# Optimization experiments

Hardware: AMD Instinct MI355X
Metric: run time of the kernel (lower is better)

Reference implementation:

```python
import jax, jax.numpy as jnp
import numpy as np

B, T, D, H, L, V, CTX = 4, 2048, 256, 8, 12, 256, 2048
HD = D // H


def _ln(x, w, b, eps=1e-5):
    m = x.mean(-1, keepdims=True)
    v = ((x - m) ** 2).mean(-1, keepdims=True)
    return (x - m) * jax.lax.rsqrt(v + eps) * w + b


def setup_inputs() -> dict:
    key = jax.random.key(0)
    ks = jax.random.split(key, 16)
    s = 0.02
    inp = {
        "x": jax.random.randint(ks[0], (B, T), 0, V, dtype=jnp.int32),
        "tok_embed": jax.random.normal(ks[1], (V, D), jnp.float32) * s,
        "pos_embed": jax.random.normal(ks[2], (CTX, D), jnp.float32) * s,
        # stacked per-layer params (leading axis = layer)
        "ln1_w": jnp.ones((L, D), jnp.float32),
        "ln1_b": jnp.zeros((L, D), jnp.float32),
        "qkv_w": jax.random.normal(ks[3], (L, D, 3 * D), jnp.float32) * s,
        "qkv_b": jnp.zeros((L, 3 * D), jnp.float32),
        "out_w": jax.random.normal(ks[4], (L, D, D), jnp.float32) * s,
        "out_b": jnp.zeros((L, D), jnp.float32),
        "ln2_w": jnp.ones((L, D), jnp.float32),
        "ln2_b": jnp.zeros((L, D), jnp.float32),
        "fc1_w": jax.random.normal(ks[5], (L, D, 4 * D), jnp.float32) * s,
        "fc1_b": jnp.zeros((L, 4 * D), jnp.float32),
        "fc2_w": jax.random.normal(ks[6], (L, 4 * D, D), jnp.float32) * s,
        "fc2_b": jnp.zeros((L, D), jnp.float32),
        "lnf_w": jnp.ones((D,), jnp.float32),
        "lnf_b": jnp.zeros((D,), jnp.float32),
        "head_w": jax.random.normal(ks[7], (D, V), jnp.float32) * s,
        "head_b": jnp.zeros((V,), jnp.float32),
    }
    return inp


def _forward(x, tok_embed, pos_embed, ln1_w, ln1_b, qkv_w, qkv_b, out_w, out_b,
             ln2_w, ln2_b, fc1_w, fc1_b, fc2_w, fc2_b, lnf_w, lnf_b, head_w, head_b):
    Tcur = x.shape[1]
    h = tok_embed[x] + pos_embed[:Tcur][None, :, :]  # (B,T,D)
    causal = jnp.triu(jnp.ones((Tcur, Tcur), bool), k=1)  # True above diagonal
    scale = jnp.sqrt(jnp.asarray(HD, h.dtype))

    def step(h, p):
        (l1w, l1b, qw, qb, ow, ob, l2w, l2b, f1w, f1b, f2w, f2b) = p
        # attention
        z = _ln(h, l1w, l1b)
        qkv = z @ qw + qb  # (B,T,3D)
        qkv = qkv.reshape(h.shape[0], Tcur, 3, H, HD)
        q, k, v = qkv[:, :, 0], qkv[:, :, 1], qkv[:, :, 2]  # (B,T,H,HD)
        attn = jnp.einsum('bqhd,bkhd->bhqk', q, k) / scale
        attn = jnp.where(causal, -jnp.inf, attn)
        attn = jax.nn.softmax(attn, axis=-1)
        o = jnp.einsum('bhqk,bkhd->bqhd', attn, v).reshape(h.shape[0], Tcur, D)
        h = h + o @ ow + ob
        # MLP (torch nn.GELU default = exact erf gelu)
        z = _ln(h, l2w, l2b)
        z = jax.nn.gelu(z @ f1w + f1b, approximate=False)
        h = h + z @ f2w + f2b
        return h, None

    params = (ln1_w, ln1_b, qkv_w, qkv_b, out_w, out_b,
              ln2_w, ln2_b, fc1_w, fc1_b, fc2_w, fc2_b)
    h, _ = jax.lax.scan(step, h, params)
    h = _ln(h, lnf_w, lnf_b)
    return h @ head_w + head_b  # (B,T,V)


def reference(x, tok_embed, pos_embed, ln1_w, ln1_b, qkv_w, qkv_b, out_w, out_b,
              ln2_w, ln2_b, fc1_w, fc1_b, fc2_w, fc2_b, lnf_w, lnf_b, head_w, head_b):
    return _forward(x, tok_embed, pos_embed, ln1_w, ln1_b, qkv_w, qkv_b, out_w, out_b,
                    ln2_w, ln2_b, fc1_w, fc1_b, fc2_w, fc2_b, lnf_w, lnf_b, head_w, head_b)
```

## Files before the change

kernel.cpp:

```cpp
#include <hip/hip_runtime.h>
#include <cstdint>

#define TT 2048
#define DD 256
#define HH 8
#define LL 12

typedef __attribute__((ext_vector_type(8))) short s16x8;
typedef __attribute__((ext_vector_type(4))) float f32x4;

__device__ __forceinline__ unsigned short f2bf(float f) {
  union { float f; unsigned u; } v; v.f = f;
  return (unsigned short)((v.u + 0x7FFFu + ((v.u >> 16) & 1u)) >> 16);
}

__device__ __forceinline__ unsigned cvtpk(float lo, float hi) {
  unsigned r;
  asm("v_cvt_pk_bf16_f32 %0, %1, %2" : "=v"(r) : "v"(lo), "v"(hi));
  return r;
}

__device__ __forceinline__ float geluf(float x) {
  return 0.5f * x * (1.0f + erff(x * 0.70710678118654752f));
}

__device__ __forceinline__ float fexp2(float x) {
  float r;
  asm("v_exp_f32 %0, %1" : "=v"(r) : "v"(x));
  return r;
}

__device__ __forceinline__ void gload16(const void* g, void* l) {
  __builtin_amdgcn_global_load_lds((const __attribute__((address_space(1))) unsigned int*)g,
                                   (__attribute__((address_space(3))) unsigned int*)l, 16, 0, 0);
}

__global__ __launch_bounds__(256) void k_embed(const int* __restrict__ x,
                                               const float* __restrict__ tok,
                                               const float* __restrict__ pos,
                                               float* __restrict__ h) {
  int i = blockIdx.x * 256 + threadIdx.x;
  int row = i >> 6, c = i & 63;
  int t = x[row];
  f32x4 tv = ((const f32x4*)(tok + (size_t)t * DD))[c];
  f32x4 pv = ((const f32x4*)(pos + (size_t)(row & (TT - 1)) * DD))[c];
  ((f32x4*)(h + (size_t)row * DD))[c] = tv + pv;
}

__global__ __launch_bounds__(256) void k_ln(const float* __restrict__ h,
                                            const float* __restrict__ wgt,
                                            const float* __restrict__ bia,
                                            unsigned short* __restrict__ z) {
  int row = blockIdx.x * 4 + (threadIdx.x >> 6);
  int lane = threadIdx.x & 63;
  f32x4 v = ((const f32x4*)(h + (size_t)row * DD))[lane];
  float s = v[0] + v[1] + v[2] + v[3];
#pragma unroll
  for (int m = 32; m; m >>= 1) s += __shfl_xor(s, m);
  float mean = s * (1.0f / DD);
  f32x4 d = v - mean;
  float s2 = d[0] * d[0] + d[1] * d[1] + d[2] * d[2] + d[3] * d[3];
#pragma unroll
  for (int m = 32; m; m >>= 1) s2 += __shfl_xor(s2, m);
  float inv = rsqrtf(s2 * (1.0f / DD) + 1e-5f);
  f32x4 wv = ((const f32x4*)wgt)[lane];
  f32x4 bv = ((const f32x4*)bia)[lane];
  float o0 = d[0] * inv * wv[0] + bv[0], o1 = d[1] * inv * wv[1] + bv[1];
  float o2 = d[2] * inv * wv[2] + bv[2], o3 = d[3] * inv * wv[3] + bv[3];
  unsigned long long u64 = (unsigned long long)cvtpk(o0, o1) |
                           ((unsigned long long)cvtpk(o2, o3) << 32);
  *(unsigned long long*)(z + (size_t)row * DD + lane * 4) = u64;
}

__global__ __launch_bounds__(256) void k_cast_all(const float* __restrict__ qw, const float* __restrict__ ow,
                                                  const float* __restrict__ f1, const float* __restrict__ f2,
                                                  unsigned short* __restrict__ dst) {
  __shared__ float Tt[32][33];
  const int l = blockIdx.y;
  const int t = blockIdx.x;
  const float* src;
  unsigned short* d;
  int K, N, tk, tn;
  if (t < 192) {
    src = qw + (size_t)l * 196608; d = dst + (size_t)l * 786432;
    K = 256; N = 768; tk = t / 24; tn = t % 24;
  } else if (t < 256) {
    int t2 = t - 192;
    src = ow + (size_t)l * 65536; d = dst + (size_t)l * 786432 + 196608;
    K = 256; N = 256; tk = t2 >> 3; tn = t2 & 7;
  } else if (t < 512) {
    int t3 = t - 256;
    src = f1 + (size_t)l * 262144; d = dst + (size_t)l * 786432 + 262144;
    K = 256; N = 1024; tk = t3 >> 5; tn = t3 & 31;
  } else {
    int t4 = t - 512;
    src = f2 + (size_t)l * 262144; d = dst + (size_t)l * 786432 + 524288;
    K = 1024; N = 256; tk = t4 >> 3; tn = t4 & 7;
  }
  const int tx = threadIdx.x & 31, ty = threadIdx.x >> 5;
#pragma unroll
  for (int r = 0; r < 4; ++r) {
    int row = ty + r * 8;
    Tt[row][tx] = src[(size_t)(tk * 32 + row) * N + tn * 32 + tx];
  }
  __syncthreads();
#pragma unroll
  for (int r = 0; r < 4; ++r) {
    int row = ty + r * 8;
    d[(size_t)(tn * 32 + row) * K + tk * 32 + tx] = f2bf(Tt[tx][row]);
  }
}

__global__ __launch_bounds__(256) void k_cast_tr4(const float* __restrict__ qw, const float* __restrict__ ow,
                                                  const float* __restrict__ f1, const float* __restrict__ f2,
                                                  unsigned short* __restrict__ dq, unsigned short* __restrict__ dO,
                                                  unsigned short* __restrict__ d1, unsigned short* __restrict__ d2) {
  int t0 = blockIdx.x * 256 + threadIdx.x;
  int stride = gridDim.x * 256;
  for (int i = t0; i < 196608; i += stride) dq[i] = f2bf(qw[(i & 255) * 768 + (i >> 8)]);
  for (int i = t0; i < 65536; i += stride) dO[i] = f2bf(ow[(i & 255) * 256 + (i >> 8)]);
  for (int i = t0; i < 262144; i += stride) d1[i] = f2bf(f1[(i & 255) * 1024 + (i >> 8)]);
  for (int i = t0; i < 262144; i += stride) d2[i] = f2bf(f2[(i & 1023) * 256 + (i >> 10)]);
}

__global__ __launch_bounds__(256) void k_cast_tr256(const float* __restrict__ src, unsigned short* __restrict__ dst) {
  int i = blockIdx.x * 256 + threadIdx.x;
  dst[i] = f2bf(src[(i & 255) * 256 + (i >> 8)]);
}

template <int MODE, int MI>
__global__ __launch_bounds__(256, 2) void k_gemm(const unsigned short* __restrict__ A,
                                                 const unsigned short* __restrict__ BT,
                                                 const float* __restrict__ bias,
                                                 void* out, const float* resid,
                                                 int M, int N, int K) {
  __shared__ __align__(16) unsigned short As[2][MI * 32 * 64];
  __shared__ __align__(16) unsigned short Bs[2][128 * 64];
  const int tid = threadIdx.x;
  const int lane = tid & 63, wv = tid >> 6;
  const int wr = wv >> 1, wc = wv & 1;
  const int l15 = lane & 15, g = lane >> 4;
  const int BM = MI * 32;
  const int tm = blockIdx.y, tn = blockIdx.x;
  f32x4 acc[MI][4] = {};
  const int nk = K >> 6;
  const unsigned short* Ag0 = A + (size_t)tm * BM * K;
  const unsigned short* Bg0 = BT + (size_t)tn * 128 * K;
  const int srow = tid >> 3, spart = tid & 7;

#pragma unroll
  for (int it = 0; it < MI; ++it)
    gload16(Ag0 + (size_t)(it * 32 + srow) * K + spart * 8, As[0] + (it * 256 + tid) * 8);
#pragma unroll
  for (int it = 0; it < 4; ++it)
    gload16(Bg0 + (size_t)(it * 32 + srow) * K + spart * 8, Bs[0] + (it * 256 + tid) * 8);
  __syncthreads();

  int buf = 0;
  for (int kt = 0; kt < nk; ++kt) {
    const bool have_next = (kt + 1 < nk);
    if (have_next) {
#pragma unroll
      for (int it = 0; it < MI; ++it)
        gload16(Ag0 + (size_t)(it * 32 + srow) * K + (kt + 1) * 64 + spart * 8,
                As[buf ^ 1] + (it * 256 + tid) * 8);
#pragma unroll
      for (int it = 0; it < 4; ++it)
        gload16(Bg0 + (size_t)(it * 32 + srow) * K + (kt + 1) * 64 + spart * 8,
                Bs[buf ^ 1] + (it * 256 + tid) * 8);
    }
#pragma unroll
    for (int ks = 0; ks < 2; ++ks) {
      s16x8 af[MI], bf[4];
#pragma unroll
      for (int mi = 0; mi < MI; ++mi)
        af[mi] = *(const s16x8*)(As[buf] + (wr * MI * 16 + mi * 16 + l15) * 64 + ks * 32 + g * 8);
#pragma unroll
      for (int ni = 0; ni < 4; ++ni)
        bf[ni] = *(const s16x8*)(Bs[buf] + (wc * 64 + ni * 16 + l15) * 64 + ks * 32 + g * 8);
#pragma unroll
      for (int mi = 0; mi < MI; ++mi)
#pragma unroll
        for (int ni = 0; ni < 4; ++ni)
          acc[mi][ni] = __builtin_amdgcn_mfma_f32_16x16x32_bf16(af[mi], bf[ni], acc[mi][ni], 0, 0, 0);
    }
    if (have_next) {
      __syncthreads();
      buf ^= 1;
    }
  }
#pragma unroll
  for (int ni = 0; ni < 4; ++ni) {
    int col = tn * 128 + wc * 64 + ni * 16 + l15;
    float bv = bias[col];
#pragma unroll
    for (int mi = 0; mi < MI; ++mi) {
      int row0 = tm * BM + wr * MI * 16 + mi * 16 + g * 4;
#pragma unroll
      for (int r = 0; r < 4; ++r) {
        size_t idx = (size_t)(row0 + r) * N + col;
        float vvv = acc[mi][ni][r] + bv;
        if (MODE == 0) ((unsigned short*)out)[idx] = f2bf(vvv);
        else if (MODE == 1) ((unsigned short*)out)[idx] = f2bf(geluf(vvv));
        else if (MODE == 2) ((float*)out)[idx] = resid[idx] + vvv;
        else ((float*)out)[idx] = vvv;
      }
    }
  }
}

__global__ __launch_bounds__(256, 2) void k_attn(const unsigned short* __restrict__ qkv,
                                                 unsigned short* __restrict__ o) {
  __shared__ __align__(16) unsigned short Ks[2][128 * 40];
  __shared__ __align__(16) unsigned short Vs[2][2 * 32 * 72];
  __shared__ __align__(16) unsigned short Ps[4][2 * 16 * 72];
  const int tid = threadIdx.x, lane = tid & 63, w = tid >> 6;
  const int l15 = lane & 15, g = lane >> 4;
  const int p = blockIdx.x;
  const int b = blockIdx.y >> 3, hh = blockIdx.y & 7;
  const size_t base = (size_t)b * TT * 768 + hh * 32;
  const float scl2 = 0.25503492f;
  const int qt0 = p, qt1 = 31 - p;
  const int nt0 = (qt0 >> 1) + 1;
  const int kr = tid >> 1, khf = tid & 1;
  const int vk = tid & 127, vdh = tid >> 7;
  const int vkh = vk >> 6, vklo = vk & 63;
  unsigned short* Pw = &Ps[w][0];

  s16x8 qf0 = *(const s16x8*)(qkv + base + (size_t)(qt0 * 64 + w * 16 + l15) * 768 + g * 8);
  s16x8 qf1 = *(const s16x8*)(qkv + base + (size_t)(qt1 * 64 + w * 16 + l15) * 768 + g * 8);

  {
    const unsigned short* kp = qkv + base + (size_t)kr * 768 + 256 + khf * 16;
    s16x8 k0 = *(const s16x8*)kp;
    s16x8 k1 = *(const s16x8*)(kp + 8);
    const unsigned short* vp = qkv + base + (size_t)vk * 768 + 512 + vdh * 16;
    s16x8 v0 = *(const s16x8*)vp;
    s16x8 v1 = *(const s16x8*)(vp + 8);
    *(s16x8*)(Ks[0] + kr * 40 + khf * 16) = k0;
    *(s16x8*)(Ks[0] + kr * 40 + khf * 16 + 8) = k1;
    unsigned short* vb = Vs[0] + vkh * 2304;
#pragma unroll
    for (int e = 0; e < 8; ++e) {
      int d0 = vdh * 16 + e, d1 = vdh * 16 + 8 + e;
      vb[d0 * 72 + (vklo ^ (((d0 >> 3) & 3) << 4))] = (unsigned short)v0[e];
      vb[d1 * 72 + (vklo ^ (((d1 >> 3) & 3) << 4))] = (unsigned short)v1[e];
    }
  }
  __syncthreads();

  f32x4 accO[2] = {};
  float mM = -3.0e38f, ls = 0.f;

  for (int t = 0; t < 17; ++t) {
    const int buf = t & 1;
    const bool ph = (t >= nt0);
    const int qt = ph ? qt1 : qt0;
    const int j = ph ? t - nt0 : t;
    const bool have_next = (t + 1 < 17);
    s16x8 k0n, k1n, v0n, v1n;
    if (have_next) {
      const int jn = (t + 1 >= nt0) ? t + 1 - nt0 : t + 1;
      const unsigned short* kp = qkv + base + (size_t)(jn * 128 + kr) * 768 + 256 + khf * 16;
      k0n = *(const s16x8*)kp;
      k1n = *(const s16x8*)(kp + 8);
      const unsigned short* vp = qkv + base + (size_t)(jn * 128 + vk) * 768 + 512 + vdh * 16;
      v0n = *(const s16x8*)vp;
      v1n = *(const s16x8*)(vp + 8);
    }
    const int rel = qt * 64 + w * 16 - j * 128;
    const bool full = (rel >= 127);
    int cbm = (rel + 15) >> 4; if (cbm > 7) cbm = 7;
    f32x4 st[8];
#pragma unroll
    for (int cb = 0; cb < 8; ++cb)
      if (cb <= cbm) {
        s16x8 kf = *(const s16x8*)(Ks[buf] + (cb * 16 + l15) * 40 + g * 8);
        f32x4 zz = {};
        st[cb] = __builtin_amdgcn_mfma_f32_16x16x32_bf16(kf, ph ? qf1 : qf0, zz, 0, 0, 0);
      }
    float rmax = -3.0e38f;
#pragma unroll
    for (int cb = 0; cb < 8; ++cb)
      if (cb <= cbm) {
        if (!full) {
#pragma unroll
          for (int r = 0; r < 4; ++r)
            if ((cb * 16 + g * 4 + r) > rel + l15) st[cb][r] = -3.0e38f;
        }
#pragma unroll
        for (int r = 0; r < 4; ++r) rmax = fmaxf(rmax, st[cb][r]);
      }
    rmax = fmaxf(rmax, __shfl_xor(rmax, 16));
    rmax = fmaxf(rmax, __shfl_xor(rmax, 32));
    const float rs = rmax * scl2;
    float al = 1.0f;
    if (!__all(rs <= mM + 11.5f)) {
      float nm = fmaxf(mM, rs);
      al = fexp2(mM - nm);
      mM = nm;
#pragma unroll
      for (int r = 0; r < 4; ++r) {
        float aw = __shfl(al, g * 4 + r);
        accO[0][r] *= aw;
        accO[1][r] *= aw;
      }
    }
    float rsum = 0.f;
#pragma unroll
    for (int cb = 0; cb < 8; ++cb)
      if (cb <= cbm) {
        float p0 = fexp2(fmaf(st[cb][0], scl2, -mM));
        float p1 = fexp2(fmaf(st[cb][1], scl2, -mM));
        float p2 = fexp2(fmaf(st[cb][2], scl2, -mM));
        float p3 = fexp2(fmaf(st[cb][3], scl2, -mM));
        rsum += (p0 + p1) + (p2 + p3);
        unsigned long long u = (unsigned long long)cvtpk(p0, p1) |
                               ((unsigned long long)cvtpk(p2, p3) << 32);
        *(unsigned long long*)(Pw + (cb >> 2) * 1152 + l15 * 72 + (cb & 3) * 16 + g * 4) = u;
      }
    if (cbm < 7 && !(cbm & 1))
      *(unsigned long long*)(Pw + ((cbm + 1) >> 2) * 1152 + l15 * 72 + ((cbm + 1) & 3) * 16 + g * 4) = 0ULL;
    rsum += __shfl_xor(rsum, 16);
    rsum += __shfl_xor(rsum, 32);
    ls = ls * al + rsum;
    asm volatile("s_waitcnt lgkmcnt(0)" ::: "memory");
    __builtin_amdgcn_sched_barrier(0);
    const int kcm = cbm >> 1;
#pragma unroll
    for (int kc = 0; kc < 4; ++kc)
      if (kc <= kcm) {
        s16x8 pa = *(const s16x8*)(Pw + (kc >> 1) * 1152 + l15 * 72 + (kc & 1) * 32 + g * 8);
        s16x8 bv0, bv1;
#pragma unroll
        for (int hb = 0; hb < 2; ++hb) {
          const int d = hb * 16 + l15;
          const int kxr = ((kc & 1) * 32 + g * 8) ^ (((d >> 3) & 3) << 4);
          if (hb == 0) bv0 = *(const s16x8*)(Vs[buf] + (kc >> 1) * 2304 + d * 72 + kxr);
          else bv1 = *(const s16x8*)(Vs[buf] + (kc >> 1) * 2304 + d * 72 + kxr);
        }
        accO[0] = __builtin_amdgcn_mfma_f32_16x16x32_bf16(pa, bv0, accO[0], 0, 0, 0);
        accO[1] = __builtin_amdgcn_mfma_f32_16x16x32_bf16(pa, bv1, accO[1], 0, 0, 0);
      }
    if (have_next) {
      *(s16x8*)(Ks[buf ^ 1] + kr * 40 + khf * 16) = k0n;
      *(s16x8*)(Ks[buf ^ 1] + kr * 40 + khf * 16 + 8) = k1n;
      unsigned short* vb = Vs[buf ^ 1] + vkh * 2304;
#pragma unroll
      for (int e = 0; e < 8; ++e) {
        int d0 = vdh * 16 + e, d1 = vdh * 16 + 8 + e;
        vb[d0 * 72 + (vklo ^ (((d0 >> 3) & 3) << 4))] = (unsigned short)v0n[e];
        vb[d1 * 72 + (vklo ^ (((d1 >> 3) & 3) << 4))] = (unsigned short)v1n[e];
      }
      __syncthreads();
    }
    if (t == nt0 - 1) {
      float inv = 1.0f / ls;
#pragma unroll
      for (int r = 0; r < 4; ++r) {
        float lv = __shfl(inv, g * 4 + r);
        int row = qt0 * 64 + w * 16 + g * 4 + r;
        o[(size_t)(b * TT + row) * DD + hh * 32 + l15] = f2bf(accO[0][r] * lv);
        o[(size_t)(b * TT + row) * DD + hh * 32 + 16 + l15] = f2bf(accO[1][r] * lv);
      }
      accO[0] = f32x4{};
      accO[1] = f32x4{};
      mM = -3.0e38f;
      ls = 0.f;
    }
  }
  {
    float inv = 1.0f / ls;
#pragma unroll
    for (int r = 0; r < 4; ++r) {
      float lv = __shfl(inv, g * 4 + r);
      int row = qt1 * 64 + w * 16 + g * 4 + r;
      o[(size_t)(b * TT + row) * DD + hh * 32 + l15] = f2bf(accO[0][r] * lv);
      o[(size_t)(b * TT + row) * DD + hh * 32 + 16 + l15] = f2bf(accO[1][r] * lv);
    }
  }
}

extern "C" void kernel_launch(void* const* d_in, const int* in_sizes, int n_in,
                              void* d_out, int out_size, void* d_ws, size_t ws_size,
                              hipStream_t stream) {
  const int* x = (const int*)d_in[0];
  const float* tok = (const float*)d_in[1];
  const float* pos = (const float*)d_in[2];
  const float* ln1w = (const float*)d_in[3];
  const float* ln1b = (const float*)d_in[4];
  const float* qkvw = (const float*)d_in[5];
  const float* qkvb = (const float*)d_in[6];
  const float* outw = (const float*)d_in[7];
  const float* outb = (const float*)d_in[8];
  const float* ln2w = (const float*)d_in[9];
  const float* ln2b = (const float*)d_in[10];
  const float* f1w = (const float*)d_in[11];
  const float* f1b = (const float*)d_in[12];
  const float* f2w = (const float*)d_in[13];
  const float* f2b = (const float*)d_in[14];
  const float* lnfw = (const float*)d_in[15];
  const float* lnfb = (const float*)d_in[16];
  const float* hw = (const float*)d_in[17];
  const float* hb = (const float*)d_in[18];

  char* ws = (char*)d_ws;
  float* h = (float*)(ws + 0);
  unsigned short* z = (unsigned short*)(ws + 8388608);
  unsigned short* qkvB = (unsigned short*)(ws + 12582912);
  unsigned short* ob = (unsigned short*)(ws + 25165824);
  unsigned short* a1 = (unsigned short*)(ws + 29360128);
  unsigned short* wAll = (unsigned short*)(ws + 46137344);
  const bool bigws = ws_size >= 65142784ULL;
  unsigned short* wh = (unsigned short*)(ws + (bigws ? 65011712 : 47710208));

  if (bigws)
    k_cast_all<<<dim3(768, 12), dim3(256), 0, stream>>>(qkvw, outw, f1w, f2w, wAll);
  k_cast_tr256<<<dim3(256), dim3(256), 0, stream>>>(hw, wh);
  k_embed<<<dim3(2048), dim3(256), 0, stream>>>(x, tok, pos, h);

  for (int l = 0; l < LL; ++l) {
    unsigned short* wq = wAll + (size_t)(bigws ? l : 0) * 786432;
    unsigned short* wo = wq + 196608;
    unsigned short* w1 = wo + 65536;
    unsigned short* w2 = w1 + 262144;
    if (!bigws)
      k_cast_tr4<<<dim3(1024), dim3(256), 0, stream>>>(
          qkvw + (size_t)l * 196608, outw + (size_t)l * 65536,
          f1w + (size_t)l * 262144, f2w + (size_t)l * 262144, wq, wo, w1, w2);
    k_ln<<<dim3(2048), dim3(256), 0, stream>>>(h, ln1w + l * 256, ln1b + l * 256, z);
    k_gemm<0, 4><<<dim3(6, 64), dim3(256), 0, stream>>>(z, wq, qkvb + l * 768, qkvB, nullptr, 8192, 768, 256);
    k_attn<<<dim3(16, 32), dim3(256), 0, stream>>>(qkvB, ob);
    k_gemm<2, 2><<<dim3(2, 128), dim3(256), 0, stream>>>(ob, wo, outb + l * 256, h, h, 8192, 256, 256);
    k_ln<<<dim3(2048), dim3(256), 0, stream>>>(h, ln2w + l * 256, ln2b + l * 256, z);
    k_gemm<1, 4><<<dim3(8, 64), dim3(256), 0, stream>>>(z, w1, f1b + l * 1024, a1, nullptr, 8192, 1024, 256);
    k_gemm<2, 2><<<dim3(2, 128), dim3(256), 0, stream>>>(a1, w2, f2b + l * 256, h, h, 8192, 256, 1024);
  }

  k_ln<<<dim3(2048), dim3(256), 0, stream>>>(h, lnfw, lnfb, z);
  k_gemm<3, 2><<<dim3(2, 128), dim3(256), 0, stream>>>(z, wh, hb, d_out, nullptr, 8192, 256, 256);
}
```

Before: 1.529 ms.

## Fuse residual add and LayerNorm into out-proj and FC2 GEMM epilogues

```diff
diff --git a/kernel.cpp b/kernel.cpp
--- a/kernel.cpp
+++ b/kernel.cpp
@@ -129,7 +129,7 @@
 }
 
 template <int MODE, int MI>
-__global__ __launch_bounds__(256, 2) void k_gemm(const unsigned short* __restrict__ A,
+__global__ __launch_bounds__(256, 3) void k_gemm(const unsigned short* __restrict__ A,
                                                  const unsigned short* __restrict__ BT,
                                                  const float* __restrict__ bias,
                                                  void* out, const float* resid,
@@ -146,14 +146,17 @@
   const int nk = K >> 6;
   const unsigned short* Ag0 = A + (size_t)tm * BM * K;
   const unsigned short* Bg0 = BT + (size_t)tn * 128 * K;
-  const int srow = tid >> 3, spart = tid & 7;
-
-#pragma unroll
-  for (int it = 0; it < MI; ++it)
-    gload16(Ag0 + (size_t)(it * 32 + srow) * K + spart * 8, As[0] + (it * 256 + tid) * 8);
-#pragma unroll
-  for (int it = 0; it < 4; ++it)
-    gload16(Bg0 + (size_t)(it * 32 + srow) * K + spart * 8, Bs[0] + (it * 256 + tid) * 8);
+
+#pragma unroll
+  for (int it = 0; it < MI; ++it) {
+    int c = it * 256 + tid;
+    gload16(Ag0 + (size_t)(c >> 3) * K + (c & 7) * 8, As[0] + c * 8);
+  }
+#pragma unroll
+  for (int it = 0; it < 4; ++it) {
+    int c = it * 256 + tid;
+    gload16(Bg0 + (size_t)(c >> 3) * K + (c & 7) * 8, Bs[0] + c * 8);
+  }
   __syncthreads();
 
   int buf = 0;
@@ -161,13 +164,15 @@
     const bool have_next = (kt + 1 < nk);
     if (have_next) {
 #pragma unroll
-      for (int it = 0; it < MI; ++it)
-        gload16(Ag0 + (size_t)(it * 32 + srow) * K + (kt + 1) * 64 + spart * 8,
-                As[buf ^ 1] + (it * 256 + tid) * 8);
-#pragma unroll
-      for (int it = 0; it < 4; ++it)
-        gload16(Bg0 + (size_t)(it * 32 + srow) * K + (kt + 1) * 64 + spart * 8,
-                Bs[buf ^ 1] + (it * 256 + tid) * 8);
+      for (int it = 0; it < MI; ++it) {
+        int c = it * 256 + tid;
+        gload16(Ag0 + (size_t)(c >> 3) * K + (kt + 1) * 64 + (c & 7) * 8, As[buf ^ 1] + c * 8);
+      }
+#pragma unroll
+      for (int it = 0; it < 4; ++it) {
+        int c = it * 256 + tid;
+        gload16(Bg0 + (size_t)(c >> 3) * K + (kt + 1) * 64 + (c & 7) * 8, Bs[buf ^ 1] + c * 8);
+      }
     }
 #pragma unroll
     for (int ks = 0; ks < 2; ++ks) {
@@ -202,10 +207,133 @@
         float vvv = acc[mi][ni][r] + bv;
         if (MODE == 0) ((unsigned short*)out)[idx] = f2bf(vvv);
         else if (MODE == 1) ((unsigned short*)out)[idx] = f2bf(geluf(vvv));
-        else if (MODE == 2) ((float*)out)[idx] = resid[idx] + vvv;
         else ((float*)out)[idx] = vvv;
       }
     }
+  }
+}
+
+template <int NK>
+__global__ __launch_bounds__(256, 2) void k_gemm_ln(const unsigned short* __restrict__ A,
+                                                    const unsigned short* __restrict__ BT,
+                                                    const float* __restrict__ bias,
+                                                    float* __restrict__ h,
+                                                    const float* __restrict__ lnw,
+                                                    const float* __restrict__ lnb,
+                                                    unsigned short* __restrict__ z) {
+  __shared__ __align__(16) unsigned short As[2][32 * 64];
+  __shared__ __align__(16) unsigned short Bs[2][256 * 64];
+  const int tid = threadIdx.x;
+  const int lane = tid & 63, wc = tid >> 6;
+  const int l15 = lane & 15, g = lane >> 4;
+  const int tm = blockIdx.x;
+  const int K = NK * 64;
+  f32x4 acc[2][4] = {};
+  const unsigned short* Ag0 = A + (size_t)tm * 32 * K;
+
+  gload16(Ag0 + (size_t)(tid >> 3) * K + (tid & 7) * 8, As[0] + tid * 8);
+#pragma unroll
+  for (int it = 0; it < 8; ++it) {
+    int c = it * 256 + tid;
+    gload16(BT + (size_t)(c >> 3) * K + (c & 7) * 8, Bs[0] + c * 8);
+  }
+  __syncthreads();
+
+  int buf = 0;
+  for (int kt = 0; kt < NK; ++kt) {
+    const bool have_next = (kt + 1 < NK);
+    if (have_next) {
+      gload16(Ag0 + (size_t)(tid >> 3) * K + (kt + 1) * 64 + (tid & 7) * 8, As[buf ^ 1] + tid * 8);
+#pragma unroll
+      for (int it = 0; it < 8; ++it) {
+        int c = it * 256 + tid;
+        gload16(BT + (size_t)(c >> 3) * K + (kt + 1) * 64 + (c & 7) * 8, Bs[buf ^ 1] + c * 8);
+      }
+    }
+#pragma unroll
+    for (int ks = 0; ks < 2; ++ks) {
+      s16x8 af[2], bf[4];
+#pragma unroll
+      for (int mi = 0; mi < 2; ++mi)
+        af[mi] = *(const s16x8*)(As[buf] + (mi * 16 + l15) * 64 + ks * 32 + g * 8);
+#pragma unroll
+      for (int ni = 0; ni < 4; ++ni)
+        bf[ni] = *(const s16x8*)(Bs[buf] + (wc * 64 + ni * 16 + l15) * 64 + ks * 32 + g * 8);
+#pragma unroll
+      for (int mi = 0; mi < 2; ++mi)
+#pragma unroll
+        for (int ni = 0; ni < 4; ++ni)
+          acc[mi][ni] = __builtin_amdgcn_mfma_f32_16x16x32_bf16(af[mi], bf[ni], acc[mi][ni], 0, 0, 0);
+    }
+    if (have_next) {
+      __syncthreads();
+      buf ^= 1;
+    }
+  }
+  const int row0 = tm * 32;
+  float hv[2][4][4];
+  float psum[2][4] = {}, psq[2][4] = {};
+#pragma unroll
+  for (int mi = 0; mi < 2; ++mi)
+#pragma unroll
+    for (int ni = 0; ni < 4; ++ni) {
+      int col = wc * 64 + ni * 16 + l15;
+      float bv = bias[col];
+#pragma unroll
+      for (int r = 0; r < 4; ++r) {
+        int row = row0 + mi * 16 + g * 4 + r;
+        float v = acc[mi][ni][r] + bv + h[(size_t)row * DD + col];
+        hv[mi][ni][r] = v;
+        h[(size_t)row * DD + col] = v;
+        psum[mi][r] += v;
+        psq[mi][r] += v * v;
+      }
+    }
+#pragma unroll
+  for (int m = 1; m < 16; m <<= 1)
+#pragma unroll
+    for (int mi = 0; mi < 2; ++mi)
+#pragma unroll
+      for (int r = 0; r < 4; ++r) {
+        psum[mi][r] += __shfl_xor(psum[mi][r], m);
+        psq[mi][r] += __shfl_xor(psq[mi][r], m);
+      }
+  __syncthreads();
+  float* red = (float*)&As[0][0];
+  if (l15 == 0) {
+#pragma unroll
+    for (int mi = 0; mi < 2; ++mi)
+#pragma unroll
+      for (int r = 0; r < 4; ++r) {
+        int rw = mi * 16 + g * 4 + r;
+        red[wc * 32 + rw] = psum[mi][r];
+        red[128 + wc * 32 + rw] = psq[mi][r];
+      }
+  }
+  __syncthreads();
+  float mean[2][4], inv[2][4];
+#pragma unroll
+  for (int mi = 0; mi < 2; ++mi)
+#pragma unroll
+    for (int r = 0; r < 4; ++r) {
+      int rw = mi * 16 + g * 4 + r;
+      float s = (red[rw] + red[32 + rw]) + (red[64 + rw] + red[96 + rw]);
+      float q = (red[128 + rw] + red[160 + rw]) + (red[192 + rw] + red[224 + rw]);
+      float mn = s * (1.0f / DD);
+      mean[mi][r] = mn;
+      inv[mi][r] = rsqrtf(q * (1.0f / DD) - mn * mn + 1e-5f);
+    }
+#pragma unroll
+  for (int ni = 0; ni < 4; ++ni) {
+    int col = wc * 64 + ni * 16 + l15;
+    float wv = lnw[col], bv = lnb[col];
+#pragma unroll
+    for (int mi = 0; mi < 2; ++mi)
+#pragma unroll
+      for (int r = 0; r < 4; ++r) {
+        int row = row0 + mi * 16 + g * 4 + r;
+        z[(size_t)row * DD + col] = f2bf((hv[mi][ni][r] - mean[mi][r]) * inv[mi][r] * wv + bv);
+      }
   }
 }
 
@@ -355,10 +483,10 @@
       __syncthreads();
     }
     if (t == nt0 - 1) {
-      float inv = 1.0f / ls;
-#pragma unroll
-      for (int r = 0; r < 4; ++r) {
-        float lv = __shfl(inv, g * 4 + r);
+      float invl = 1.0f / ls;
+#pragma unroll
+      for (int r = 0; r < 4; ++r) {
+        float lv = __shfl(invl, g * 4 + r);
         int row = qt0 * 64 + w * 16 + g * 4 + r;
         o[(size_t)(b * TT + row) * DD + hh * 32 + l15] = f2bf(accO[0][r] * lv);
         o[(size_t)(b * TT + row) * DD + hh * 32 + 16 + l15] = f2bf(accO[1][r] * lv);
@@ -370,10 +498,10 @@
     }
   }
   {
-    float inv = 1.0f / ls;
+    float invl = 1.0f / ls;
 #pragma unroll
     for (int r = 0; r < 4; ++r) {
-      float lv = __shfl(inv, g * 4 + r);
+      float lv = __shfl(invl, g * 4 + r);
       int row = qt1 * 64 + w * 16 + g * 4 + r;
       o[(size_t)(b * TT + row) * DD + hh * 32 + l15] = f2bf(accO[0][r] * lv);
       o[(size_t)(b * TT + row) * DD + hh * 32 + 16 + l15] = f2bf(accO[1][r] * lv);
@@ -418,6 +546,7 @@
     k_cast_all<<<dim3(768, 12), dim3(256), 0, stream>>>(qkvw, outw, f1w, f2w, wAll);
   k_cast_tr256<<<dim3(256), dim3(256), 0, stream>>>(hw, wh);
   k_embed<<<dim3(2048), dim3(256), 0, stream>>>(x, tok, pos, h);
+  k_ln<<<dim3(2048), dim3(256), 0, stream>>>(h, ln1w, ln1b, z);
 
   for (int l = 0; l < LL; ++l) {
     unsigned short* wq = wAll + (size_t)(bigws ? l : 0) * 786432;
@@ -428,15 +557,15 @@
       k_cast_tr4<<<dim3(1024), dim3(256), 0, stream>>>(
           qkvw + (size_t)l * 196608, outw + (size_t)l * 65536,
           f1w + (size_t)l * 262144, f2w + (size_t)l * 262144, wq, wo, w1, w2);
-    k_ln<<<dim3(2048), dim3(256), 0, stream>>>(h, ln1w + l * 256, ln1b + l * 256, z);
-    k_gemm<0, 4><<<dim3(6, 64), dim3(256), 0, stream>>>(z, wq, qkvb + l * 768, qkvB, nullptr, 8192, 768, 256);
+    k_gemm<0, 2><<<dim3(6, 128), dim3(256), 0, stream>>>(z, wq, qkvb + l * 768, qkvB, nullptr, 8192, 768, 256);
     k_attn<<<dim3(16, 32), dim3(256), 0, stream>>>(qkvB, ob);
-    k_gemm<2, 2><<<dim3(2, 128), dim3(256), 0, stream>>>(ob, wo, outb + l * 256, h, h, 8192, 256, 256);
-    k_ln<<<dim3(2048), dim3(256), 0, stream>>>(h, ln2w + l * 256, ln2b + l * 256, z);
-    k_gemm<1, 4><<<dim3(8, 64), dim3(256), 0, stream>>>(z, w1, f1b + l * 1024, a1, nullptr, 8192, 1024, 256);
-    k_gemm<2, 2><<<dim3(2, 128), dim3(256), 0, stream>>>(a1, w2, f2b + l * 256, h, h, 8192, 256, 1024);
-  }
-
-  k_ln<<<dim3(2048), dim3(256), 0, stream>>>(h, lnfw, lnfb, z);
+    k_gemm_ln<4><<<dim3(256), dim3(256), 0, stream>>>(ob, wo, outb + l * 256, h,
+                                                      ln2w + l * 256, ln2b + l * 256, z);
+    k_gemm<1, 2><<<dim3(8, 128), dim3(256), 0, stream>>>(z, w1, f1b + l * 1024, a1, nullptr, 8192, 1024, 256);
+    const float* nw = (l == LL - 1) ? lnfw : ln1w + (l + 1) * 256;
+    const float* nb = (l == LL - 1) ? lnfb : ln1b + (l + 1) * 256;
+    k_gemm_ln<16><<<dim3(256), dim3(256), 0, stream>>>(a1, w2, f2b + l * 256, h, nw, nb, z);
+  }
+
   k_gemm<3, 2><<<dim3(2, 128), dim3(256), 0, stream>>>(z, wh, hb, d_out, nullptr, 8192, 256, 256);
 }
```

Result: faster. 1.390 ms (-9.1%).
